# Optimization experiments

Hardware: AMD Instinct MI355X
Metric: run time of the kernel (lower is better)

Reference implementation:

```python
import jax, jax.numpy as jnp
import numpy as np

T, B, N, C = 4, 4, 4096, 512
H = 8
D = C // H            # head_dim = 64
TAU = 2.0             # LIF tau
VTH = 1.0             # LIF threshold


def lif_spike(x):
    # LIFNode called once from zero state: v = 0 + (x - 0)/tau; spike = v >= vth
    v = x / TAU
    return (v >= VTH).astype(x.dtype)


def setup_inputs() -> dict:
    key = jax.random.key(0)
    ks = jax.random.split(key, 9)
    s = 0.05  # weight scale so pre-spike potentials straddle the threshold
    x = jax.random.normal(ks[0], (T, B, N, C), dtype=jnp.float32)
    Wq = jax.random.normal(ks[1], (C, C), dtype=jnp.float32) * s
    bq = jnp.zeros((C,), dtype=jnp.float32)
    Wk = jax.random.normal(ks[2], (C, C), dtype=jnp.float32) * s
    bk = jnp.zeros((C,), dtype=jnp.float32)
    Wv = jax.random.normal(ks[3], (C, C), dtype=jnp.float32) * s
    bv = jnp.zeros((C,), dtype=jnp.float32)
    Wo = jax.random.normal(ks[4], (C, C), dtype=jnp.float32) * s
    bo = jnp.zeros((C,), dtype=jnp.float32)
    return {"x": x, "Wq": Wq, "bq": bq, "Wk": Wk, "bk": bk,
            "Wv": Wv, "bv": bv, "Wo": Wo, "bo": bo}


def reference(x, Wq, bq, Wk, bk, Wv, bv, Wo, bo):
    # nn.Linear: y = x @ W.T + b (SeqToANNContainer just flattens (T,B))
    q = jnp.einsum('tbnc,oc->tbno', x, Wq) + bq
    k = jnp.einsum('tbnc,oc->tbno', x, Wk) + bk
    v = jnp.einsum('tbnc,oc->tbno', x, Wv) + bv
    # reshape to heads; attention runs over the spiking time axis T per token
    q = q.reshape(T, B, N, H, D).transpose(1, 2, 0, 3, 4)   # (B,N,T,H,D)
    k = k.reshape(T, B, N, H, D).transpose(1, 2, 3, 4, 0)   # (B,N,H,D,T)
    v = v.reshape(T, B, N, H, D).transpose(1, 2, 3, 0, 4)   # (B,N,H,T,D)
    attn = jnp.einsum('bnthd,bnhds->bnths', q, k) / jnp.sqrt(jnp.float32(D))
    attn = lif_spike(attn)                                  # binary spikes replace softmax
    out = jnp.einsum('bnths,bnhsd->bnthd', attn, v)         # (B,N,T,H,D)
    out = out.transpose(2, 0, 1, 3, 4).reshape(T, B, N, C)
    return jnp.einsum('tbnc,oc->tbno', out, Wo) + bo
```

## Files before the change

kernel.cpp:

```cpp
#include <hip/hip_runtime.h>

#define PTOT  16384
#define CCC   512
#define HHH   8
#define NK1   32
#define NK2   16

typedef __attribute__((ext_vector_type(4)))  float f32x4;
typedef __attribute__((ext_vector_type(16))) float f32x16;
typedef _Float16 half_t;
typedef __attribute__((ext_vector_type(8))) _Float16 f16x8;

#define MFMA16(a,b,c) __builtin_amdgcn_mfma_f32_16x16x32_f16(a,b,c,0,0,0)
#define MFMA32(a,b,c) __builtin_amdgcn_mfma_f32_32x32x16_f16(a,b,c,0,0,0)

#define XH_OFF   ((size_t)0)
#define XL_OFF   ((size_t)33554432)
#define ACT_OFF  ((size_t)67108864)
#define W_OFF    ((size_t)100663296)
#define WPL      ((size_t)262144)

__device__ __forceinline__ size_t blk_off16(int row, int col) {
    return ((size_t)((row >> 4) * 16 + (col >> 5)) << 9)
         + (size_t)(((((col >> 3) & 3) * 16) + (row & 15)) << 3) + (col & 7);
}
__device__ __forceinline__ size_t blk_off32(int row, int k) {
    return ((size_t)((row >> 5) * 32 + (k >> 4)) << 9)
         + (size_t)(((((k >> 3) & 1) * 32) + (row & 31)) << 3) + (k & 7);
}

__global__ void k0_split(const float* __restrict__ x,
                         const float* __restrict__ Wq, const float* __restrict__ Wk,
                         const float* __restrict__ Wv, const float* __restrict__ Wo,
                         half_t* __restrict__ ws)
{
    const int u = blockIdx.x * 256 + threadIdx.x;
    const float* src;
    half_t *dh, *dl;
    int row, c;
    bool old16 = false;
    if (u < 4194304) {
        row = u >> 6; c = u & 63;
        src = x; dh = ws + XH_OFF; dl = ws + XL_OFF;
    } else {
        const int u2 = u - 4194304;
        const int mat = u2 >> 15, r = u2 & 32767;
        row = r >> 6; c = r & 63;
        if      (mat == 0) { src = Wq; dh = ws + W_OFF;         dl = ws + W_OFF + WPL; }
        else if (mat == 1) { src = Wk; dh = ws + W_OFF + 2*WPL; dl = ws + W_OFF + 3*WPL; }
        else if (mat == 2) { src = Wv; dh = ws + W_OFF + 4*WPL; dl = nullptr; }
        else               { src = Wo; dh = ws + W_OFF + 5*WPL; dl = nullptr; old16 = true; }
    }
    const int k = c * 8;
    const float4 a = *(const float4*)(src + (size_t)row * CCC + k);
    const float4 b = *(const float4*)(src + (size_t)row * CCC + k + 4);
    const float e[8] = {a.x, a.y, a.z, a.w, b.x, b.y, b.z, b.w};
    f16x8 vh8, vl8;
    #pragma unroll
    for (int d = 0; d < 8; ++d) {
        const half_t hi = (half_t)e[d];
        const half_t lo = (half_t)(e[d] - (float)hi);
        vh8[d] = hi; vl8[d] = lo;
    }
    const size_t off = old16 ? blk_off16(row, k) : blk_off32(row, k);
    *(f16x8*)(dh + off) = vh8;
    if (dl) *(f16x8*)(dl + off) = vl8;
}

__global__ __launch_bounds__(256, 3)
void k1_mfma(const half_t* __restrict__ ws,
             const float* __restrict__ bq, const float* __restrict__ bk,
             const float* __restrict__ bv,
             half_t* __restrict__ acth)
{
    __shared__ __align__(16) char smem[52224];

    const int tid  = threadIdx.x;
    const int lane = tid & 63;
    const int wv   = tid >> 6;
    const int rg   = wv >> 1;
    const int cg   = wv & 1;
    const int l31  = lane & 31;
    const int l5   = lane >> 5;

    const int xcd  = blockIdx.x & 7;
    const int rest = blockIdx.x >> 3;
    const int h    = rest & 7;
    const int tg   = rest >> 3;
    const int p0   = (tg * 8 + xcd) * 32;

    const int cnt  = (wv < 2) ? 5 : 4;
    const int base = (wv < 2) ? wv * 5 : 2 + wv * 4;
    const half_t* gb[5]; int lo_[5];
    #pragma unroll
    for (int ii = 0; ii < 5; ++ii) {
        const int i = base + ii;
        size_t eoff; int loff;
        if (i < 8) {
            const int t = i >> 1, pl = i & 1;
            const size_t rbg = (size_t)t * 512 + (p0 >> 5);
            eoff = (pl ? XL_OFF : XH_OFF) + rbg * 16384 + lane * 8;
            loff = i * 1024;
        } else {
            const int s = (i - 8) & 15;
            const int plw = (s >> 1) > 4 ? 4 : (s >> 1), cb = s & 1;
            eoff = W_OFF + (size_t)plw * WPL + (size_t)(h * 2 + cb) * 16384 + lane * 8;
            loff = 8192 + s * 1024;
        }
        gb[ii] = ws + eoff;
        lo_[ii] = loff;
    }

#define K1_STAGE(buf, kt) do {                                                  \
    _Pragma("unroll")                                                           \
    for (int ii = 0; ii < 5; ++ii)                                              \
        if (ii < cnt)                                                           \
            __builtin_amdgcn_global_load_lds(                                   \
                (const __attribute__((address_space(1))) void*)(gb[ii] + (size_t)(kt) * 512), \
                (__attribute__((address_space(3))) void*)(smem + (buf) * 18432 + lo_[ii]),    \
                16, 0, 0);                                                      \
    } while (0)

    f32x16 accQ[2], accK[2], accV[2];
    {
        const int c0 = h * 64 + cg * 32 + l31;
        const float q0 = bq[c0], k0 = bk[c0], v0 = bv[c0];
        #pragma unroll
        for (int i = 0; i < 16; ++i) {
            accQ[0][i] = q0; accQ[1][i] = q0;
            accK[0][i] = k0; accK[1][i] = k0;
            accV[0][i] = v0; accV[1][i] = v0;
        }
    }

    K1_STAGE(0, 0);

    #pragma unroll 2
    for (int kt = 0; kt < NK1; ++kt) {
        const int cur = kt & 1;
        if (kt + 1 < NK1) {
            K1_STAGE(cur ^ 1, kt + 1);
            if (cnt == 5) asm volatile("s_waitcnt vmcnt(5)" ::: "memory");
            else          asm volatile("s_waitcnt vmcnt(4)" ::: "memory");
        } else {
            asm volatile("s_waitcnt vmcnt(0)" ::: "memory");
        }
        __builtin_amdgcn_sched_barrier(0);
        __builtin_amdgcn_s_barrier();

        const char* bp = smem + cur * 18432;
        const int boff = 8192 + cg * 1024 + lane * 16;
        const f16x8 Bqh = *(const f16x8*)(bp + boff);
        const f16x8 Bql = *(const f16x8*)(bp + boff + 2048);
        const f16x8 Bkh = *(const f16x8*)(bp + boff + 4096);
        const f16x8 Bkl = *(const f16x8*)(bp + boff + 6144);
        const f16x8 Bvh = *(const f16x8*)(bp + boff + 8192);
        f16x8 Ah[2], Al[2];
        #pragma unroll
        for (int rf = 0; rf < 2; ++rf) {
            const int t = rg * 2 + rf;
            Ah[rf] = *(const f16x8*)(bp + (t * 2 + 0) * 1024 + lane * 16);
            Al[rf] = *(const f16x8*)(bp + (t * 2 + 1) * 1024 + lane * 16);
        }
        accQ[0] = MFMA32(Ah[0], Bqh, accQ[0]);
        accQ[1] = MFMA32(Ah[1], Bqh, accQ[1]);
        accK[0] = MFMA32(Ah[0], Bkh, accK[0]);
        accK[1] = MFMA32(Ah[1], Bkh, accK[1]);
        accV[0] = MFMA32(Ah[0], Bvh, accV[0]);
        accV[1] = MFMA32(Ah[1], Bvh, accV[1]);
        accQ[0] = MFMA32(Ah[0], Bql, accQ[0]);
        accQ[1] = MFMA32(Ah[1], Bql, accQ[1]);
        accK[0] = MFMA32(Ah[0], Bkl, accK[0]);
        accK[1] = MFMA32(Ah[1], Bkl, accK[1]);
        accQ[0] = MFMA32(Al[0], Bqh, accQ[0]);
        accQ[1] = MFMA32(Al[1], Bqh, accQ[1]);
        accK[0] = MFMA32(Al[0], Bkh, accK[0]);
        accK[1] = MFMA32(Al[1], Bkh, accK[1]);

        asm volatile("s_waitcnt lgkmcnt(0)" ::: "memory");
        __builtin_amdgcn_s_barrier();
        __builtin_amdgcn_sched_barrier(0);
    }

    float* qa = (float*)smem;
    float* ka = qa + 4352;
    float* va = qa + 8704;

    const int ar  = tid >> 2;
    const int t_  = ar >> 4;
    const int jj  = ar & 15;
    const int sub = tid & 3;

    #pragma unroll
    for (int hh = 0; hh < 2; ++hh) {
        #pragma unroll
        for (int rf = 0; rf < 2; ++rf) {
            const int t = rg * 2 + rf;
            #pragma unroll
            for (int rr = 0; rr < 8; ++rr) {
                const int reg = hh * 8 + rr;
                const int j2  = (rr & 3) + 8 * (rr >> 2) + 4 * l5;
                const int idx = (t * 16 + j2) * 68 + cg * 32 + l31;
                qa[idx] = accQ[rf][reg];
                ka[idx] = accK[rf][reg];
                va[idx] = accV[rf][reg];
            }
        }
        __syncthreads();

        const float* qp = qa + ar * 68 + sub * 16;
        const float4 q0 = *(const float4*)(qp);
        const float4 q1 = *(const float4*)(qp + 4);
        const float4 q2 = *(const float4*)(qp + 8);
        const float4 q3 = *(const float4*)(qp + 12);
        float sc[4];
        #pragma unroll
        for (int ss = 0; ss < 4; ++ss) {
            const float* kp = ka + (ss * 16 + jj) * 68 + sub * 16;
            const float4 k0 = *(const float4*)(kp);
            const float4 k1 = *(const float4*)(kp + 4);
            const float4 k2 = *(const float4*)(kp + 8);
            const float4 k3 = *(const float4*)(kp + 12);
            float p = q0.x*k0.x + q0.y*k0.y + q0.z*k0.z + q0.w*k0.w
                    + q1.x*k1.x + q1.y*k1.y + q1.z*k1.z + q1.w*k1.w
                    + q2.x*k2.x + q2.y*k2.y + q2.z*k2.z + q2.w*k2.w
                    + q3.x*k3.x + q3.y*k3.y + q3.z*k3.z + q3.w*k3.w;
            p += __shfl_xor(p, 1);
            p += __shfl_xor(p, 2);
            sc[ss] = p;
        }
        float o[16];
        #pragma unroll
        for (int d = 0; d < 16; ++d) o[d] = 0.f;
        #pragma unroll
        for (int ss = 0; ss < 4; ++ss) {
            if (sc[ss] >= 16.0f) {
                const float* vp = va + (ss * 16 + jj) * 68 + sub * 16;
                const float4 v0 = *(const float4*)(vp);
                const float4 v1 = *(const float4*)(vp + 4);
                const float4 v2 = *(const float4*)(vp + 8);
                const float4 v3 = *(const float4*)(vp + 12);
                o[0]+=v0.x; o[1]+=v0.y; o[2]+=v0.z;  o[3]+=v0.w;
                o[4]+=v1.x; o[5]+=v1.y; o[6]+=v1.z;  o[7]+=v1.w;
                o[8]+=v2.x; o[9]+=v2.y; o[10]+=v2.z; o[11]+=v2.w;
                o[12]+=v3.x;o[13]+=v3.y;o[14]+=v3.z; o[15]+=v3.w;
            }
        }
        f16x8 o0, o1;
        #pragma unroll
        for (int d = 0; d < 8; ++d) { o0[d] = (half_t)o[d]; o1[d] = (half_t)o[d + 8]; }
        const int grow = t_ * 1024 + (p0 >> 4) + hh;
        const int colb = h * 64 + sub * 16;
        const size_t cbase = ((size_t)(grow * 16 + (colb >> 5))) << 9;
        const int c0 = (colb >> 3) & 3;
        *(f16x8*)(acth + cbase + (size_t)((c0       * 16 + jj) << 3)) = o0;
        *(f16x8*)(acth + cbase + (size_t)(((c0 + 1) * 16 + jj) << 3)) = o1;
        __syncthreads();
    }
#undef K1_STAGE
}

__global__ __launch_bounds__(256, 4)
void k2_gemm(const half_t* __restrict__ acth, const half_t* __restrict__ oh,
             const float* __restrict__ bo, float* __restrict__ out)
{
    __shared__ __align__(16) char smem[32768];

    const int tid  = threadIdx.x;
    const int lane = tid & 63;
    const int wv   = tid >> 6;
    const int wr   = wv >> 1, wc = wv & 1;
    const int l15  = lane & 15, l4 = lane >> 4;
    const int bn   = (blockIdx.x & 3) * 128;
    const int bm   = (blockIdx.x >> 2) * 128;

    const half_t* gb[4]; int lo_[4];
    #pragma unroll
    for (int ii = 0; ii < 4; ++ii) {
        const int i = wv * 4 + ii;
        if (i < 8) {
            const int grow = (bm >> 4) + i;
            gb[ii] = acth + ((size_t)grow << 13) + lane * 8;
            lo_[ii] = i * 1024;
        } else {
            const int fb = i - 8;
            const int grow = (bn >> 4) + fb;
            gb[ii] = oh + ((size_t)grow << 13) + lane * 8;
            lo_[ii] = 8192 + fb * 1024;
        }
    }

#define K2_STAGE(buf, kt) do {                                                  \
    _Pragma("unroll")                                                           \
    for (int ii = 0; ii < 4; ++ii)                                              \
        __builtin_amdgcn_global_load_lds(                                       \
            (const __attribute__((address_space(1))) void*)(gb[ii] + (size_t)(kt) * 512), \
            (__attribute__((address_space(3))) void*)(smem + (buf) * 16384 + lo_[ii]),    \
            16, 0, 0);                                                          \
    } while (0)

    f32x4 acc[4][4];
    #pragma unroll
    for (int rf = 0; rf < 4; ++rf)
        #pragma unroll
        for (int cf = 0; cf < 4; ++cf) acc[rf][cf] = f32x4{0.f, 0.f, 0.f, 0.f};

    K2_STAGE(0, 0);

    #pragma unroll
    for (int kt = 0; kt < NK2; ++kt) {
        const int cur = kt & 1;
        if (kt + 1 < NK2) {
            K2_STAGE(cur ^ 1, kt + 1);
            asm volatile("s_waitcnt vmcnt(4)" ::: "memory");
        } else {
            asm volatile("s_waitcnt vmcnt(0)" ::: "memory");
        }
        __builtin_amdgcn_sched_barrier(0);
        __builtin_amdgcn_s_barrier();

        const char* bp = smem + cur * 16384;
        f16x8 B[4];
        #pragma unroll
        for (int cf = 0; cf < 4; ++cf)
            B[cf] = *(const f16x8*)(bp + 8192 + (wc * 4 + cf) * 1024 + lane * 16);
        #pragma unroll
        for (int rf = 0; rf < 4; ++rf) {
            const f16x8 A = *(const f16x8*)(bp + (wr * 4 + rf) * 1024 + lane * 16);
            #pragma unroll
            for (int cf = 0; cf < 4; ++cf)
                acc[rf][cf] = MFMA16(A, B[cf], acc[rf][cf]);
        }
        asm volatile("s_waitcnt lgkmcnt(0)" ::: "memory");
        __builtin_amdgcn_s_barrier();
        __builtin_amdgcn_sched_barrier(0);
    }

    float bo4[4];
    #pragma unroll
    for (int cf = 0; cf < 4; ++cf) bo4[cf] = bo[bn + (wc * 4 + cf) * 16 + l15];

    #pragma unroll
    for (int rf = 0; rf < 4; ++rf) {
        const int row0 = bm + (wr * 4 + rf) * 16 + l4 * 4;
        #pragma unroll
        for (int cf = 0; cf < 4; ++cf) {
            const int col = bn + (wc * 4 + cf) * 16 + l15;
            #pragma unroll
            for (int r = 0; r < 4; ++r)
                out[(size_t)(row0 + r) * CCC + col] = acc[rf][cf][r] + bo4[cf];
        }
    }
#undef K2_STAGE
}

extern "C" void kernel_launch(void* const* d_in, const int* in_sizes, int n_in,
                              void* d_out, int out_size, void* d_ws, size_t ws_size,
                              hipStream_t stream)
{
    const float* x  = (const float*)d_in[0];
    const float* Wq = (const float*)d_in[1];
    const float* bq = (const float*)d_in[2];
    const float* Wk = (const float*)d_in[3];
    const float* bk = (const float*)d_in[4];
    const float* Wv = (const float*)d_in[5];
    const float* bv = (const float*)d_in[6];
    const float* Wo = (const float*)d_in[7];
    const float* bo = (const float*)d_in[8];

    half_t* ws   = (half_t*)d_ws;
    half_t* acth = ws + ACT_OFF;
    float*  out  = (float*)d_out;

    hipLaunchKernelGGL(k0_split, dim3(16896), dim3(256), 0, stream,
                       x, Wq, Wk, Wv, Wo, ws);
    hipLaunchKernelGGL(k1_mfma, dim3(4096), dim3(256), 0, stream,
                       ws, bq, bk, bv, acth);
    hipLaunchKernelGGL(k2_gemm, dim3(2048), dim3(256), 0, stream,
                       acth, ws + W_OFF + 5*WPL, bo, out);
}
```

Baseline: 388.6 us.

## Replace LDS staging with direct global-to-register double-buffered fragment loads

Both GEMM kernels stop staging tiles through shared memory with global_load_lds and barriers. Each wave now loads its MFMA fragments straight from global memory into registers, using a two-deep register double buffer, which removes the per-step s_barrier synchronisation and LDS traffic. The split kernel is reorganised to write fragment-ready layouts that make these direct loads coalesced, and launch bounds are lowered to allow more registers. The cost is that tiles shared between waves are now fetched redundantly from global memory or L2 rather than once per block, and higher register pressure lowers occupancy.

```diff
diff --git a/kernel.cpp b/kernel.cpp
--- a/kernel.cpp
+++ b/kernel.cpp
@@ -23,10 +23,6 @@
 __device__ __forceinline__ size_t blk_off16(int row, int col) {
     return ((size_t)((row >> 4) * 16 + (col >> 5)) << 9)
          + (size_t)(((((col >> 3) & 3) * 16) + (row & 15)) << 3) + (col & 7);
-}
-__device__ __forceinline__ size_t blk_off32(int row, int k) {
-    return ((size_t)((row >> 5) * 32 + (k >> 4)) << 9)
-         + (size_t)(((((k >> 3) & 1) * 32) + (row & 31)) << 3) + (k & 7);
 }
 
 __global__ void k0_split(const float* __restrict__ x,
@@ -35,39 +31,61 @@
                          half_t* __restrict__ ws)
 {
     const int u = blockIdx.x * 256 + threadIdx.x;
-    const float* src;
-    half_t *dh, *dl;
-    int row, c;
-    bool old16 = false;
     if (u < 4194304) {
-        row = u >> 6; c = u & 63;
-        src = x; dh = ws + XH_OFF; dl = ws + XL_OFF;
-    } else {
-        const int u2 = u - 4194304;
-        const int mat = u2 >> 15, r = u2 & 32767;
-        row = r >> 6; c = r & 63;
-        if      (mat == 0) { src = Wq; dh = ws + W_OFF;         dl = ws + W_OFF + WPL; }
-        else if (mat == 1) { src = Wk; dh = ws + W_OFF + 2*WPL; dl = ws + W_OFF + 3*WPL; }
-        else if (mat == 2) { src = Wv; dh = ws + W_OFF + 4*WPL; dl = nullptr; }
-        else               { src = Wo; dh = ws + W_OFF + 5*WPL; dl = nullptr; old16 = true; }
-    }
-    const int k = c * 8;
-    const float4 a = *(const float4*)(src + (size_t)row * CCC + k);
-    const float4 b = *(const float4*)(src + (size_t)row * CCC + k + 4);
+        const int f = u >> 6, lane6 = u & 63;
+        const int grow32 = f >> 5, ktc = f & 31;
+        const int row = grow32 * 32 + (lane6 & 31);
+        const int k   = ktc * 16 + (lane6 >> 5) * 8;
+        const float4 a = *(const float4*)(x + (size_t)row * CCC + k);
+        const float4 b = *(const float4*)(x + (size_t)row * CCC + k + 4);
+        const float e[8] = {a.x, a.y, a.z, a.w, b.x, b.y, b.z, b.w};
+        f16x8 vh8, vl8;
+        #pragma unroll
+        for (int d = 0; d < 8; ++d) {
+            const half_t hi = (half_t)e[d];
+            vh8[d] = hi; vl8[d] = (half_t)(e[d] - (float)hi);
+        }
+        const size_t off = ((size_t)f << 9) + lane6 * 8;
+        *(f16x8*)(ws + XH_OFF + off) = vh8;
+        *(f16x8*)(ws + XL_OFF + off) = vl8;
+        return;
+    }
+    const int u2  = u - 4194304;
+    const int mat = u2 >> 15, r = u2 & 32767;
+    if (mat < 3) {
+        const float* src = (mat == 0) ? Wq : (mat == 1) ? Wk : Wv;
+        const int f = r >> 6, lane6 = r & 63;
+        const int grow32 = f >> 5, ktc = f & 31;
+        const int row = grow32 * 32 + (lane6 & 31);
+        const int k   = ktc * 16 + (lane6 >> 5) * 8;
+        const float4 a = *(const float4*)(src + (size_t)row * CCC + k);
+        const float4 b = *(const float4*)(src + (size_t)row * CCC + k + 4);
+        const float e[8] = {a.x, a.y, a.z, a.w, b.x, b.y, b.z, b.w};
+        f16x8 vh8, vl8;
+        #pragma unroll
+        for (int d = 0; d < 8; ++d) {
+            const half_t hi = (half_t)e[d];
+            vh8[d] = hi; vl8[d] = (half_t)(e[d] - (float)hi);
+        }
+        const size_t off = ((size_t)f << 9) + lane6 * 8;
+        half_t* dh = ws + W_OFF + (size_t)(mat * 2) * WPL;
+        *(f16x8*)(dh + off) = vh8;
+        if (mat < 2) *(f16x8*)(dh + WPL + off) = vl8;
+        return;
+    }
+    const int gr = r >> 10, v = r & 1023;
+    const int ktc = v >> 6, chunk = (v >> 4) & 3, i = v & 15;
+    const int row = gr * 16 + i, col = ktc * 32 + chunk * 8;
+    const float4 a = *(const float4*)(Wo + (size_t)row * CCC + col);
+    const float4 b = *(const float4*)(Wo + (size_t)row * CCC + col + 4);
     const float e[8] = {a.x, a.y, a.z, a.w, b.x, b.y, b.z, b.w};
-    f16x8 vh8, vl8;
-    #pragma unroll
-    for (int d = 0; d < 8; ++d) {
-        const half_t hi = (half_t)e[d];
-        const half_t lo = (half_t)(e[d] - (float)hi);
-        vh8[d] = hi; vl8[d] = lo;
-    }
-    const size_t off = old16 ? blk_off16(row, k) : blk_off32(row, k);
-    *(f16x8*)(dh + off) = vh8;
-    if (dl) *(f16x8*)(dl + off) = vl8;
-}
-
-__global__ __launch_bounds__(256, 3)
+    f16x8 vh8;
+    #pragma unroll
+    for (int d = 0; d < 8; ++d) vh8[d] = (half_t)e[d];
+    *(f16x8*)(ws + W_OFF + 5 * WPL + blk_off16(row, col)) = vh8;
+}
+
+__global__ __launch_bounds__(256, 2)
 void k1_mfma(const half_t* __restrict__ ws,
              const float* __restrict__ bq, const float* __restrict__ bk,
              const float* __restrict__ bv,
@@ -89,37 +107,20 @@
     const int tg   = rest >> 3;
     const int p0   = (tg * 8 + xcd) * 32;
 
-    const int cnt  = (wv < 2) ? 5 : 4;
-    const int base = (wv < 2) ? wv * 5 : 2 + wv * 4;
-    const half_t* gb[5]; int lo_[5];
-    #pragma unroll
-    for (int ii = 0; ii < 5; ++ii) {
-        const int i = base + ii;
-        size_t eoff; int loff;
-        if (i < 8) {
-            const int t = i >> 1, pl = i & 1;
-            const size_t rbg = (size_t)t * 512 + (p0 >> 5);
-            eoff = (pl ? XL_OFF : XH_OFF) + rbg * 16384 + lane * 8;
-            loff = i * 1024;
-        } else {
-            const int s = (i - 8) & 15;
-            const int plw = (s >> 1) > 4 ? 4 : (s >> 1), cb = s & 1;
-            eoff = W_OFF + (size_t)plw * WPL + (size_t)(h * 2 + cb) * 16384 + lane * 8;
-            loff = 8192 + s * 1024;
-        }
-        gb[ii] = ws + eoff;
-        lo_[ii] = loff;
-    }
-
-#define K1_STAGE(buf, kt) do {                                                  \
-    _Pragma("unroll")                                                           \
-    for (int ii = 0; ii < 5; ++ii)                                              \
-        if (ii < cnt)                                                           \
-            __builtin_amdgcn_global_load_lds(                                   \
-                (const __attribute__((address_space(1))) void*)(gb[ii] + (size_t)(kt) * 512), \
-                (__attribute__((address_space(3))) void*)(smem + (buf) * 18432 + lo_[ii]),    \
-                16, 0, 0);                                                      \
-    } while (0)
+    const half_t* pA[2][2];
+    #pragma unroll
+    for (int rb = 0; rb < 2; ++rb) {
+        const size_t grow = (size_t)(rg * 2 + rb) * 512 + (p0 >> 5);
+        pA[rb][0] = ws + XH_OFF + (grow << 14) + lane * 8;
+        pA[rb][1] = ws + XL_OFF + (grow << 14) + lane * 8;
+    }
+    const half_t* pB[5];
+    {
+        const size_t grB = (size_t)(h * 2 + cg) << 14;
+        #pragma unroll
+        for (int s = 0; s < 5; ++s)
+            pB[s] = ws + W_OFF + (size_t)s * WPL + grB + lane * 8;
+    }
 
     f32x16 accQ[2], accK[2], accV[2];
     {
@@ -133,53 +134,44 @@
         }
     }
 
-    K1_STAGE(0, 0);
-
-    #pragma unroll 2
-    for (int kt = 0; kt < NK1; ++kt) {
-        const int cur = kt & 1;
-        if (kt + 1 < NK1) {
-            K1_STAGE(cur ^ 1, kt + 1);
-            if (cnt == 5) asm volatile("s_waitcnt vmcnt(5)" ::: "memory");
-            else          asm volatile("s_waitcnt vmcnt(4)" ::: "memory");
-        } else {
-            asm volatile("s_waitcnt vmcnt(0)" ::: "memory");
-        }
-        __builtin_amdgcn_sched_barrier(0);
-        __builtin_amdgcn_s_barrier();
-
-        const char* bp = smem + cur * 18432;
-        const int boff = 8192 + cg * 1024 + lane * 16;
-        const f16x8 Bqh = *(const f16x8*)(bp + boff);
-        const f16x8 Bql = *(const f16x8*)(bp + boff + 2048);
-        const f16x8 Bkh = *(const f16x8*)(bp + boff + 4096);
-        const f16x8 Bkl = *(const f16x8*)(bp + boff + 6144);
-        const f16x8 Bvh = *(const f16x8*)(bp + boff + 8192);
-        f16x8 Ah[2], Al[2];
-        #pragma unroll
-        for (int rf = 0; rf < 2; ++rf) {
-            const int t = rg * 2 + rf;
-            Ah[rf] = *(const f16x8*)(bp + (t * 2 + 0) * 1024 + lane * 16);
-            Al[rf] = *(const f16x8*)(bp + (t * 2 + 1) * 1024 + lane * 16);
-        }
-        accQ[0] = MFMA32(Ah[0], Bqh, accQ[0]);
-        accQ[1] = MFMA32(Ah[1], Bqh, accQ[1]);
-        accK[0] = MFMA32(Ah[0], Bkh, accK[0]);
-        accK[1] = MFMA32(Ah[1], Bkh, accK[1]);
-        accV[0] = MFMA32(Ah[0], Bvh, accV[0]);
-        accV[1] = MFMA32(Ah[1], Bvh, accV[1]);
-        accQ[0] = MFMA32(Ah[0], Bql, accQ[0]);
-        accQ[1] = MFMA32(Ah[1], Bql, accQ[1]);
-        accK[0] = MFMA32(Ah[0], Bkl, accK[0]);
-        accK[1] = MFMA32(Ah[1], Bkl, accK[1]);
-        accQ[0] = MFMA32(Al[0], Bqh, accQ[0]);
-        accQ[1] = MFMA32(Al[1], Bqh, accQ[1]);
-        accK[0] = MFMA32(Al[0], Bkh, accK[0]);
-        accK[1] = MFMA32(Al[1], Bkh, accK[1]);
-
-        asm volatile("s_waitcnt lgkmcnt(0)" ::: "memory");
-        __builtin_amdgcn_s_barrier();
-        __builtin_amdgcn_sched_barrier(0);
+    f16x8 Ab[2][2][2], Bb[2][5];
+
+#define K1_LOADSET(buf, kt) do {                                               \
+    _Pragma("unroll")                                                          \
+    for (int rb = 0; rb < 2; ++rb) {                                           \
+        Ab[buf][rb][0] = *(const f16x8*)(pA[rb][0] + (size_t)(kt) * 512);      \
+        Ab[buf][rb][1] = *(const f16x8*)(pA[rb][1] + (size_t)(kt) * 512);      \
+    }                                                                          \
+    _Pragma("unroll")                                                          \
+    for (int s = 0; s < 5; ++s)                                                \
+        Bb[buf][s] = *(const f16x8*)(pB[s] + (size_t)(kt) * 512);              \
+    } while (0)
+
+#define K1_MM(buf) do {                                                        \
+    accQ[0] = MFMA32(Ab[buf][0][0], Bb[buf][0], accQ[0]);                      \
+    accQ[1] = MFMA32(Ab[buf][1][0], Bb[buf][0], accQ[1]);                      \
+    accK[0] = MFMA32(Ab[buf][0][0], Bb[buf][2], accK[0]);                      \
+    accK[1] = MFMA32(Ab[buf][1][0], Bb[buf][2], accK[1]);                      \
+    accV[0] = MFMA32(Ab[buf][0][0], Bb[buf][4], accV[0]);                      \
+    accV[1] = MFMA32(Ab[buf][1][0], Bb[buf][4], accV[1]);                      \
+    accQ[0] = MFMA32(Ab[buf][0][0], Bb[buf][1], accQ[0]);                      \
+    accQ[1] = MFMA32(Ab[buf][1][0], Bb[buf][1], accQ[1]);                      \
+    accK[0] = MFMA32(Ab[buf][0][0], Bb[buf][3], accK[0]);                      \
+    accK[1] = MFMA32(Ab[buf][1][0], Bb[buf][3], accK[1]);                      \
+    accQ[0] = MFMA32(Ab[buf][0][1], Bb[buf][0], accQ[0]);                      \
+    accQ[1] = MFMA32(Ab[buf][1][1], Bb[buf][0], accQ[1]);                      \
+    accK[0] = MFMA32(Ab[buf][0][1], Bb[buf][2], accK[0]);                      \
+    accK[1] = MFMA32(Ab[buf][1][1], Bb[buf][2], accK[1]);                      \
+    } while (0)
+
+    K1_LOADSET(0, 0);
+    K1_LOADSET(1, 1);
+    #pragma unroll
+    for (int kt = 0; kt < NK1; kt += 2) {
+        K1_MM(0);
+        if (kt + 2 < NK1) K1_LOADSET(0, kt + 2);
+        K1_MM(1);
+        if (kt + 3 < NK1) K1_LOADSET(1, kt + 3);
     }
 
     float* qa = (float*)smem;
@@ -257,15 +249,14 @@
         *(f16x8*)(acth + cbase + (size_t)(((c0 + 1) * 16 + jj) << 3)) = o1;
         __syncthreads();
     }
-#undef K1_STAGE
-}
-
-__global__ __launch_bounds__(256, 4)
+#undef K1_LOADSET
+#undef K1_MM
+}
+
+__global__ __launch_bounds__(256, 3)
 void k2_gemm(const half_t* __restrict__ acth, const half_t* __restrict__ oh,
              const float* __restrict__ bo, float* __restrict__ out)
 {
-    __shared__ __align__(16) char smem[32768];
-
     const int tid  = threadIdx.x;
     const int lane = tid & 63;
     const int wv   = tid >> 6;
@@ -274,66 +265,45 @@
     const int bn   = (blockIdx.x & 3) * 128;
     const int bm   = (blockIdx.x >> 2) * 128;
 
-    const half_t* gb[4]; int lo_[4];
-    #pragma unroll
-    for (int ii = 0; ii < 4; ++ii) {
-        const int i = wv * 4 + ii;
-        if (i < 8) {
-            const int grow = (bm >> 4) + i;
-            gb[ii] = acth + ((size_t)grow << 13) + lane * 8;
-            lo_[ii] = i * 1024;
-        } else {
-            const int fb = i - 8;
-            const int grow = (bn >> 4) + fb;
-            gb[ii] = oh + ((size_t)grow << 13) + lane * 8;
-            lo_[ii] = 8192 + fb * 1024;
-        }
-    }
-
-#define K2_STAGE(buf, kt) do {                                                  \
-    _Pragma("unroll")                                                           \
-    for (int ii = 0; ii < 4; ++ii)                                              \
-        __builtin_amdgcn_global_load_lds(                                       \
-            (const __attribute__((address_space(1))) void*)(gb[ii] + (size_t)(kt) * 512), \
-            (__attribute__((address_space(3))) void*)(smem + (buf) * 16384 + lo_[ii]),    \
-            16, 0, 0);                                                          \
+    const half_t* pA[4]; const half_t* pB[4];
+    #pragma unroll
+    for (int f = 0; f < 4; ++f) {
+        pA[f] = acth + ((size_t)((bm >> 4) + wr * 4 + f) << 13) + lane * 8;
+        pB[f] = oh   + ((size_t)((bn >> 4) + wc * 4 + f) << 13) + lane * 8;
+    }
+
+    f32x4 acc[4][4];
+    #pragma unroll
+    for (int rf = 0; rf < 4; ++rf)
+        #pragma unroll
+        for (int cf = 0; cf < 4; ++cf) acc[rf][cf] = f32x4{0.f, 0.f, 0.f, 0.f};
+
+    f16x8 Ab[2][4], Bb[2][4];
+
+#define K2_LOADSET(buf, kt) do {                                               \
+    _Pragma("unroll")                                                          \
+    for (int f = 0; f < 4; ++f) {                                              \
+        Ab[buf][f] = *(const f16x8*)(pA[f] + (size_t)(kt) * 512);              \
+        Bb[buf][f] = *(const f16x8*)(pB[f] + (size_t)(kt) * 512);              \
+    }                                                                          \
     } while (0)
 
-    f32x4 acc[4][4];
-    #pragma unroll
-    for (int rf = 0; rf < 4; ++rf)
-        #pragma unroll
-        for (int cf = 0; cf < 4; ++cf) acc[rf][cf] = f32x4{0.f, 0.f, 0.f, 0.f};
-
-    K2_STAGE(0, 0);
-
-    #pragma unroll
-    for (int kt = 0; kt < NK2; ++kt) {
-        const int cur = kt & 1;
-        if (kt + 1 < NK2) {
-            K2_STAGE(cur ^ 1, kt + 1);
-            asm volatile("s_waitcnt vmcnt(4)" ::: "memory");
-        } else {
-            asm volatile("s_waitcnt vmcnt(0)" ::: "memory");
-        }
-        __builtin_amdgcn_sched_barrier(0);
-        __builtin_amdgcn_s_barrier();
-
-        const char* bp = smem + cur * 16384;
-        f16x8 B[4];
-        #pragma unroll
-        for (int cf = 0; cf < 4; ++cf)
-            B[cf] = *(const f16x8*)(bp + 8192 + (wc * 4 + cf) * 1024 + lane * 16);
-        #pragma unroll
-        for (int rf = 0; rf < 4; ++rf) {
-            const f16x8 A = *(const f16x8*)(bp + (wr * 4 + rf) * 1024 + lane * 16);
-            #pragma unroll
-            for (int cf = 0; cf < 4; ++cf)
-                acc[rf][cf] = MFMA16(A, B[cf], acc[rf][cf]);
-        }
-        asm volatile("s_waitcnt lgkmcnt(0)" ::: "memory");
-        __builtin_amdgcn_s_barrier();
-        __builtin_amdgcn_sched_barrier(0);
+#define K2_MM(buf) do {                                                        \
+    _Pragma("unroll")                                                          \
+    for (int rf = 0; rf < 4; ++rf)                                             \
+        _Pragma("unroll")                                                      \
+        for (int cf = 0; cf < 4; ++cf)                                         \
+            acc[rf][cf] = MFMA16(Ab[buf][rf], Bb[buf][cf], acc[rf][cf]);       \
+    } while (0)
+
+    K2_LOADSET(0, 0);
+    K2_LOADSET(1, 1);
+    #pragma unroll
+    for (int kt = 0; kt < NK2; kt += 2) {
+        K2_MM(0);
+        if (kt + 2 < NK2) K2_LOADSET(0, kt + 2);
+        K2_MM(1);
+        if (kt + 3 < NK2) K2_LOADSET(1, kt + 3);
     }
 
     float bo4[4];
@@ -351,7 +321,8 @@
                 out[(size_t)(row0 + r) * CCC + col] = acc[rf][cf][r] + bo4[cf];
         }
     }
-#undef K2_STAGE
+#undef K2_LOADSET
+#undef K2_MM
 }
 
 extern "C" void kernel_launch(void* const* d_in, const int* in_sizes, int n_in,
```

New measurement: 431.5 us. 11.1% more time.
